# Performance work log

Hardware: AMD Instinct MI355X
Metric: run time of the kernel (lower is better)

Reference implementation:

```python
import jax, jax.numpy as jnp
import numpy as np
import math

C = 512         # embed_size
L_V = 196       # num_patches (square -> no cls token)
B_V = 64        # image batch
B_T = 32        # caption batch
N_WORD = 24     # words per caption (all cap_lens equal)
SPARSE_RATIO = 0.5
AGGR_RATIO = 0.5
NUM_KEEP = math.ceil(L_V * SPARSE_RATIO)            # 98 kept tokens
KEEPED = int(L_V * AGGR_RATIO * SPARSE_RATIO)       # 49 aggregated tokens
HIDDEN = int(C * 0.2)                               # 102 MLP hidden (dim_ratio=0.2)
LAMBDA = 4.0                                        # xattn softmax temperature
LN_EPS = 1e-5


def l2norm(x, axis=-1):
    n = jnp.linalg.norm(x, axis=axis, keepdims=True)
    return x / jnp.maximum(n, 1e-12)


def setup_inputs() -> dict:
    key = jax.random.key(0)
    ks = jax.random.split(key, 4)
    img_embs = jax.random.normal(ks[0], (B_V, L_V, C), dtype=jnp.float32)
    cap_embs = jax.random.normal(ks[1], (B_T, N_WORD, C), dtype=jnp.float32)
    cap_lens = jnp.full((B_T,), N_WORD, dtype=jnp.int64 if jax.config.read('jax_enable_x64') else jnp.int32)
    # TokenAggregation params: LayerNorm -> Linear(C,HIDDEN) -> GELU -> Linear(HIDDEN,KEEPED), scale
    ln_gamma = jnp.ones((C,), jnp.float32)
    ln_beta = jnp.zeros((C,), jnp.float32)
    W1 = jax.random.normal(ks[2], (C, HIDDEN), dtype=jnp.float32) * 0.02
    b1 = jnp.zeros((HIDDEN,), jnp.float32)
    W2 = jax.random.normal(ks[3], (HIDDEN, KEEPED), dtype=jnp.float32) * 0.02
    b2 = jnp.zeros((KEEPED,), jnp.float32)
    scale = jnp.ones((), jnp.float32)
    return dict(img_embs=img_embs, cap_embs=cap_embs, cap_lens=cap_lens,
                ln_gamma=ln_gamma, ln_beta=ln_beta, W1=W1, b1=b1, W2=W2, b2=b2, scale=scale)


def _forward(img_embs, cap_embs, ln_gamma, ln_beta, W1, b1, W2, b2, scale):
    # --- global attention scores (computed under no_grad in torch) ---
    img_norm = l2norm(img_embs)                                   # (Bv,Lv,C)
    cap_norm = l2norm(cap_embs)                                   # (Bt,W,C)
    img_glo = l2norm(jnp.mean(img_embs, axis=1, keepdims=True))   # (Bv,1,C)
    self_attn = jnp.sum(img_glo * img_norm, axis=-1)              # (Bv,Lv)
    cap_glo = l2norm(jnp.mean(cap_embs, axis=1))                  # (Bt,C)
    cross_attn = jnp.einsum('tc,vlc->tvl', cap_glo, img_norm)     # (Bt,Bv,Lv)
    score = jax.lax.stop_gradient(self_attn[None] + cross_attn)   # (Bt,Bv,Lv)

    # --- TokenSparse: sort, split keep / non-keep ---
    order = jnp.argsort(-score, axis=-1)                          # descending indices
    score_sort = jnp.take_along_axis(score, order, axis=-1)
    keep_idx = order[..., :NUM_KEEP]                              # (Bt,Bv,K)
    non_idx = order[..., NUM_KEEP:]                               # (Bt,Bv,Lv-K)
    rank = jnp.argsort(order, axis=-1)                            # inverse permutation
    score_mask = (rank < NUM_KEEP).astype(score.dtype)            # (Bt,Bv,Lv)

    bidx = jnp.arange(B_V)[None, :, None]
    select_tokens = img_embs[bidx, keep_idx]                      # (Bt,Bv,K,C) gather
    non_tokens = img_embs[bidx, non_idx]                          # (Bt,Bv,Lv-K,C)
    non_w = jax.nn.softmax(score_sort[..., NUM_KEEP:], axis=-1)   # (Bt,Bv,Lv-K)
    extra_token = jnp.sum(non_tokens * non_w[..., None], axis=-2, keepdims=True)  # (Bt,Bv,1,C)

    # --- TokenAggregation: LN -> MLP -> softmax -> bmm ---
    mu = jnp.mean(select_tokens, axis=-1, keepdims=True)
    var = jnp.var(select_tokens, axis=-1, keepdims=True)
    xn = (select_tokens - mu) * jax.lax.rsqrt(var + LN_EPS) * ln_gamma + ln_beta
    h = jax.nn.gelu(jnp.einsum('tvkc,ch->tvkh', xn, W1) + b1, approximate=False)
    w = jnp.einsum('tvkh,hp->tvkp', h, W2) + b2                   # (Bt,Bv,K,P)
    w = jnp.swapaxes(w, -1, -2) * scale                           # (Bt,Bv,P,K)
    w = jax.nn.softmax(w, axis=-1)
    aggr = jnp.einsum('tvpk,tvkc->tvpc', w, select_tokens)        # (Bt,Bv,P,C)

    keep_tokens = jnp.concatenate([aggr, extra_token], axis=2)    # (Bt,Bv,P+1,C)
    sel_norm = l2norm(keep_tokens)

    # --- mask_xattn_one_text: SCAN-style t2i attention ---
    sims = jnp.einsum('twc,tvpc->tvwp', cap_norm, sel_norm)       # (Bt,Bv,W,P+1)
    attn = jax.nn.softmax(LAMBDA * sims, axis=-1)
    ctx = l2norm(jnp.einsum('tvwp,tvpc->tvwc', attn, sel_norm))   # (Bt,Bv,W,C)
    word_sim = jnp.einsum('twc,tvwc->tvw', cap_norm, ctx)         # (Bt,Bv,W)
    sim = jnp.mean(word_sim, axis=-1)                             # (Bt,Bv)
    improve_sims = sim.T                                          # (Bv,Bt)
    return improve_sims, score_mask


def reference(img_embs, cap_embs, cap_lens, ln_gamma, ln_beta, W1, b1, W2, b2, scale):
    # cap_lens are all N_WORD (constant), so the per-caption loop is fully vectorized.
    return _forward(img_embs, cap_embs, ln_gamma, ln_beta, W1, b1, W2, b2, scale)
```

## Files before the change

### kernel.cpp

```cpp
#include <hip/hip_runtime.h>
#include <hip/hip_bf16.h>
#include <math.h>

#define CDIM 512
#define LV 196
#define BV 64
#define BT 32
#define NW 24
#define NKEEP 98
#define NNON 98
#define KEEPED 49
#define HID 102
#define LAMBDA_ 4.0f
#define LN_EPS_ 1e-5f

#define WS_CAPNORM 0
#define WS_CAPGLO  (WS_CAPNORM + BT*NW*CDIM)
#define WS_IMGGLO  (WS_CAPGLO + BT*CDIM)
#define WS_INVN    (WS_IMGGLO + BV*CDIM)
#define WS_WLOG    (WS_INVN + BV*LV)
#define WS_SCORE   (WS_WLOG + BV*LV*KEEPED)
#define WS_END     (WS_SCORE + BT*BV*LV)
#define WS_IMGT_B  ((size_t)WS_END * 4)
#define TOKPAD 224
#define WS_NEED_B  (WS_IMGT_B + (size_t)BV * CDIM * TOKPAD * 2)
#define WS_W1T_B   ((size_t)WS_SCORE * 4)
#define WS_W2T_B   (WS_W1T_B + (size_t)112 * 512 * 2)

typedef short v8s __attribute__((ext_vector_type(8)));
typedef float v4f __attribute__((ext_vector_type(4)));
#define MFMA16(a, b, c) __builtin_amdgcn_mfma_f32_16x16x32_bf16((a), (b), (c), 0, 0, 0)

#define WA_STR 232
#define TOK_STR 40
#define SEL_STR 520
#define G_STR 66
#define XN_STR 520
#define HB_STR 136

#define SELQ_STR 136
#define CAPQ_STR 136
#define K4_SMEM   51968
#define OFF_SEL   0
#define OFF_WA    19216
#define OFF_CAPQ  19216
#define OFF_SIMS  19216
#define OFF_G     27408
#define OFF_SC    48912
#define OFF_KIDX  49696
#define OFF_NIDX  50088
#define OFF_CNT   50480
#define OFF_WK    50496
#define OFF_RED   50896
#define OFF_POOL2 51408
#define OFF_INV   51664

__device__ __forceinline__ ushort bfb(float f) {
  __hip_bfloat16 h = __float2bfloat16(f);
  union { __hip_bfloat16 h; ushort u; } cv; cv.h = h; return cv.u;
}

__global__ __launch_bounds__(512) void k0_prep(const float* __restrict__ img,
                                               const float* __restrict__ W1,
                                               const float* __restrict__ W2,
                                               float* __restrict__ ws) {
  int v = blockIdx.x, kt = blockIdx.y, c = threadIdx.x;
  if (kt == 7) {
    if (v < 56) {
      #pragma unroll
      for (int r = 0; r < 2; ++r) {
        int h = v * 2 + r;
        float val = (h < HID) ? W1[(size_t)c * HID + h] : 0.f;
        ((ushort*)((char*)ws + WS_W1T_B))[(size_t)h * 512 + c] = bfb(val);
      }
    } else {
      for (int e = c; e < 1024; e += 512) {
        int idx = (v - 56) * 1024 + e;
        int p = idx >> 7, h = idx & 127;
        float val = (p < KEEPED && h < HID) ? W2[(size_t)h * KEEPED + p] : 0.f;
        ((ushort*)((char*)ws + WS_W2T_B))[(size_t)p * 128 + h] = bfb(val);
      }
    }
    return;
  }
  float x[32];
  #pragma unroll
  for (int kk = 0; kk < 32; ++kk) {
    int tok = kt * 32 + kk;
    x[kk] = (tok < LV) ? img[((size_t)v * LV + tok) * CDIM + c] : 0.f;
  }
  __hip_bfloat16* imgT = (__hip_bfloat16*)((char*)ws + WS_IMGT_B);
  uint* dst = (uint*)(imgT + ((size_t)v * CDIM + c) * TOKPAD + kt * 32);
  #pragma unroll
  for (int g = 0; g < 4; ++g) {
    uint4 u;
    u.x = (uint)bfb(x[g*8+0]) | ((uint)bfb(x[g*8+1]) << 16);
    u.y = (uint)bfb(x[g*8+2]) | ((uint)bfb(x[g*8+3]) << 16);
    u.z = (uint)bfb(x[g*8+4]) | ((uint)bfb(x[g*8+5]) << 16);
    u.w = (uint)bfb(x[g*8+6]) | ((uint)bfb(x[g*8+7]) << 16);
    *(uint4*)(dst + g * 4) = u;
  }
}

__global__ __launch_bounds__(512) void k5_prep(const float* __restrict__ W1,
                                               const float* __restrict__ W2,
                                               float* __restrict__ ws) {
  int b = blockIdx.x, tid = threadIdx.x;
  if (b < 112) {
    int h = b;
    float val = (h < HID) ? W1[(size_t)tid * HID + h] : 0.f;
    ((ushort*)((char*)ws + WS_W1T_B))[(size_t)h * 512 + tid] = bfb(val);
  } else {
    int p = b - 112;
    if (tid < 128) {
      int h = tid;
      float val = (p < KEEPED && h < HID) ? W2[(size_t)h * KEEPED + p] : 0.f;
      ((ushort*)((char*)ws + WS_W2T_B))[(size_t)p * 128 + h] = bfb(val);
    }
  }
}

__global__ __launch_bounds__(256) void k1_glo(const float* __restrict__ img,
                                              const float* __restrict__ cap,
                                              float* __restrict__ ws) {
  __shared__ float red[256];
  __shared__ float s_part[4 * CDIM];
  __shared__ float s_glo[CDIM];
  int b = blockIdx.x, tid = threadIdx.x;
  if (b < BT) {
    int t = b;
    int wv = tid >> 6, lane = tid & 63;
    int cb = lane * 8;
    float4 sA = make_float4(0.f,0.f,0.f,0.f), sB = make_float4(0.f,0.f,0.f,0.f);
    for (int w = wv; w < NW; w += 4) {
      const float* p = cap + ((size_t)t * NW + w) * CDIM + cb;
      float4 xa = *(const float4*)p;
      float4 xb = *(const float4*)(p + 4);
      float ss = xa.x*xa.x + xa.y*xa.y + xa.z*xa.z + xa.w*xa.w
               + xb.x*xb.x + xb.y*xb.y + xb.z*xb.z + xb.w*xb.w;
      #pragma unroll
      for (int off = 32; off > 0; off >>= 1) ss += __shfl_xor(ss, off, 64);
      float inv = 1.f / fmaxf(sqrtf(ss), 1e-12f);
      float* q = ws + WS_CAPNORM + ((size_t)t * NW + w) * CDIM + cb;
      *(float4*)q       = make_float4(xa.x*inv, xa.y*inv, xa.z*inv, xa.w*inv);
      *(float4*)(q + 4) = make_float4(xb.x*inv, xb.y*inv, xb.z*inv, xb.w*inv);
      sA.x += xa.x; sA.y += xa.y; sA.z += xa.z; sA.w += xa.w;
      sB.x += xb.x; sB.y += xb.y; sB.z += xb.z; sB.w += xb.w;
    }
    *(float4*)&s_part[wv * CDIM + cb]     = sA;
    *(float4*)&s_part[wv * CDIM + cb + 4] = sB;
    __syncthreads();
    if (tid < 128) {
      float4 g = make_float4(0.f, 0.f, 0.f, 0.f);
      #pragma unroll
      for (int w2 = 0; w2 < 4; ++w2) {
        float4 pv = *(const float4*)&s_part[w2 * CDIM + tid * 4];
        g.x += pv.x; g.y += pv.y; g.z += pv.z; g.w += pv.w;
      }
      g.x /= (float)NW; g.y /= (float)NW; g.z /= (float)NW; g.w /= (float)NW;
      *(float4*)&s_glo[tid * 4] = g;
      red[tid] = g.x*g.x + g.y*g.y + g.z*g.z + g.w*g.w;
    }
    __syncthreads();
    for (int off = 64; off > 0; off >>= 1) {
      if (tid < off) red[tid] += red[tid + off];
      __syncthreads();
    }
    float inv = 1.f / fmaxf(sqrtf(red[0]), 1e-12f);
    if (tid < 128) {
      float4 g = *(const float4*)&s_glo[tid * 4];
      *(float4*)(ws + WS_CAPGLO + (size_t)t * CDIM + tid * 4) =
          make_float4(g.x*inv, g.y*inv, g.z*inv, g.w*inv);
    }
  } else {
    int v = b - BT;
    int wv = tid >> 6, lane = tid & 63;
    int cb = lane * 8;
    const float* base = img + (size_t)v * LV * CDIM;
    float4 sA = make_float4(0.f,0.f,0.f,0.f), sB = make_float4(0.f,0.f,0.f,0.f);
    int l0 = wv * 49;
    for (int l = l0; l < l0 + 49; ++l) {
      const float* p = base + (size_t)l * CDIM + cb;
      float4 xa = *(const float4*)p;
      float4 xb = *(const float4*)(p + 4);
      sA.x += xa.x; sA.y += xa.y; sA.z += xa.z; sA.w += xa.w;
      sB.x += xb.x; sB.y += xb.y; sB.z += xb.z; sB.w += xb.w;
    }
    *(float4*)&s_part[wv * CDIM + cb]     = sA;
    *(float4*)&s_part[wv * CDIM + cb + 4] = sB;
    __syncthreads();
    if (tid < 128) {
      float4 g = make_float4(0.f, 0.f, 0.f, 0.f);
      #pragma unroll
      for (int w2 = 0; w2 < 4; ++w2) {
        float4 pv = *(const float4*)&s_part[w2 * CDIM + tid * 4];
        g.x += pv.x; g.y += pv.y; g.z += pv.z; g.w += pv.w;
      }
      g.x /= (float)LV; g.y /= (float)LV; g.z /= (float)LV; g.w /= (float)LV;
      *(float4*)&s_glo[tid * 4] = g;
      red[tid] = g.x*g.x + g.y*g.y + g.z*g.z + g.w*g.w;
    }
    __syncthreads();
    for (int off = 64; off > 0; off >>= 1) {
      if (tid < off) red[tid] += red[tid + off];
      __syncthreads();
    }
    float inv = 1.f / fmaxf(sqrtf(red[0]), 1e-12f);
    if (tid < 128) {
      float4 g = *(const float4*)&s_glo[tid * 4];
      *(float4*)(ws + WS_IMGGLO + (size_t)v * CDIM + tid * 4) =
          make_float4(g.x*inv, g.y*inv, g.z*inv, g.w*inv);
    }
  }
}

__global__ __launch_bounds__(512, 4) void k2_mlp(const float* __restrict__ img,
                                                 const float* __restrict__ gamma,
                                                 const float* __restrict__ beta,
                                                 const float* __restrict__ b1,
                                                 const float* __restrict__ b2,
                                                 float* __restrict__ ws) {
  __shared__ __align__(16) __hip_bfloat16 s_xn[32 * XN_STR];
  __hip_bfloat16* s_hb = s_xn;

  int v = blockIdx.x, seg = blockIdx.y;
  int l0 = seg * 28;
  int tid = threadIdx.x, wv = tid >> 6, lane = tid & 63;
  int quad = lane >> 4, l15 = lane & 15, koff = quad * 8;
  const __hip_bfloat16* W1T = (const __hip_bfloat16*)((const char*)ws + WS_W1T_B);
  const __hip_bfloat16* W2T = (const __hip_bfloat16*)((const char*)ws + WS_W2T_B);

  int cb = lane * 8;
  float4 g4a = *(const float4*)(gamma + cb);
  float4 g4b = *(const float4*)(gamma + cb + 4);
  float4 b4a = *(const float4*)(beta + cb);
  float4 b4b = *(const float4*)(beta + cb + 4);
  for (int tok = wv; tok < 28; tok += 8) {
    const float* p = img + ((size_t)v * LV + l0 + tok) * CDIM + cb;
    float4 xa = *(const float4*)p;
    float4 xb = *(const float4*)(p + 4);
    float s  = xa.x + xa.y + xa.z + xa.w + xb.x + xb.y + xb.z + xb.w;
    float sq = xa.x*xa.x + xa.y*xa.y + xa.z*xa.z + xa.w*xa.w
             + xb.x*xb.x + xb.y*xb.y + xb.z*xb.z + xb.w*xb.w;
    #pragma unroll
    for (int off = 32; off > 0; off >>= 1) { s += __shfl_xor(s, off, 64); sq += __shfl_xor(sq, off, 64); }
    float mean = s / (float)CDIM;
    float var = sq / (float)CDIM - mean * mean;
    float rstd = 1.f / sqrtf(var + LN_EPS_);
    if (lane == 0) ws[WS_INVN + (size_t)v * LV + l0 + tok] = 1.f / fmaxf(sqrtf(sq), 1e-12f);
    float f[8];
    f[0] = (xa.x - mean) * rstd * g4a.x + b4a.x;
    f[1] = (xa.y - mean) * rstd * g4a.y + b4a.y;
    f[2] = (xa.z - mean) * rstd * g4a.z + b4a.z;
    f[3] = (xa.w - mean) * rstd * g4a.w + b4a.w;
    f[4] = (xb.x - mean) * rstd * g4b.x + b4b.x;
    f[5] = (xb.y - mean) * rstd * g4b.y + b4b.y;
    f[6] = (xb.z - mean) * rstd * g4b.z + b4b.z;
    f[7] = (xb.w - mean) * rstd * g4b.w + b4b.w;
    uint4 u;
    u.x = (uint)bfb(f[0]) | ((uint)bfb(f[1]) << 16);
    u.y = (uint)bfb(f[2]) | ((uint)bfb(f[3]) << 16);
    u.z = (uint)bfb(f[4]) | ((uint)bfb(f[5]) << 16);
    u.w = (uint)bfb(f[6]) | ((uint)bfb(f[7]) << 16);
    *(uint4*)(s_xn + (size_t)tok * XN_STR + cb) = u;
  }
  __syncthreads();

  v4f c1[2];
  int mt_[2], nt_[2];
  #pragma unroll
  for (int i = 0; i < 2; ++i) {
    int idx = wv + 8 * i; if (idx > 13) idx = 13;
    mt_[i] = idx / 7; nt_[i] = idx % 7;
    c1[i] = (v4f){0.f, 0.f, 0.f, 0.f};
  }
  for (int ks = 0; ks < 16; ++ks) {
    #pragma unroll
    for (int i = 0; i < 2; ++i) {
      v8s a  = *(const v8s*)(s_xn + (size_t)(mt_[i] * 16 + l15) * XN_STR + ks * 32 + koff);
      v8s bb = *(const v8s*)(W1T + (size_t)(nt_[i] * 16 + l15) * 512 + ks * 32 + koff);
      c1[i] = MFMA16(a, bb, c1[i]);
    }
  }
  __syncthreads();

  #pragma unroll
  for (int i = 0; i < 2; ++i) {
    int idx = wv + 8 * i;
    if (idx < 14) {
      int h = nt_[i] * 16 + l15;
      float bias = (h < HID) ? b1[h] : 0.f;
      #pragma unroll
      for (int reg = 0; reg < 4; ++reg) {
        int row = mt_[i] * 16 + quad * 4 + reg;
        float x = c1[i][reg] + bias;
        float gl = (h < HID) ? 0.5f * x * (1.f + erff(x * 0.70710678118654752f)) : 0.f;
        s_hb[(size_t)row * HB_STR + h] = __float2bfloat16(gl);
      }
    }
  }
  for (int i = tid; i < 32 * 16; i += 512)
    s_hb[(size_t)(i >> 4) * HB_STR + 112 + (i & 15)] = __float2bfloat16(0.f);
  __syncthreads();

  int m2 = wv >> 2, n2 = wv & 3;
  v4f c2 = (v4f){0.f, 0.f, 0.f, 0.f};
  for (int ks = 0; ks < 4; ++ks) {
    v8s a  = *(const v8s*)(s_hb + (size_t)(m2 * 16 + l15) * HB_STR + ks * 32 + koff);
    v8s bb = *(const v8s*)(W2T + (size_t)(n2 * 16 + l15) * 128 + ks * 32 + koff);
    c2 = MFMA16(a, bb, c2);
  }
  {
    int p = n2 * 16 + l15;
    if (p < KEEPED) {
      float bias = b2[p];
      #pragma unroll
      for (int reg = 0; reg < 4; ++reg) {
        int tok = m2 * 16 + quad * 4 + reg;
        if (tok < 28)
          ws[WS_WLOG + ((size_t)v * LV + l0 + tok) * KEEPED + p] = c2[reg] + bias;
      }
    }
  }
}

__global__ __launch_bounds__(512) void k3_score(const float* __restrict__ img,
                                                float* __restrict__ ws) {
  __shared__ float qt[33 * 64];
  __shared__ float xt[64 * 65];
  __shared__ float dself[64];
  int v = blockIdx.x;
  int t0 = blockIdx.y * 64;
  int tid = threadIdx.x;
  int tloc = tid & 63, qg = tid >> 6;
  float acc[5];
  #pragma unroll
  for (int i = 0; i < 5; ++i) acc[i] = 0.f;
  const float* capglo = ws + WS_CAPGLO;
  const float* imgglo = ws + WS_IMGGLO + (size_t)v * CDIM;

  for (int ct = 0; ct < 8; ++ct) {
    for (int i = tid; i < 33 * 64; i += 512) {
      int q = i >> 6, cc = i & 63;
      qt[i] = (q < 32) ? capglo[(size_t)q * CDIM + ct * 64 + cc] : imgglo[ct * 64 + cc];
    }
    for (int i = tid; i < 64 * 64; i += 512) {
      int tok = i >> 6, cc = i & 63;
      int l = t0 + tok;
      xt[tok * 65 + cc] = (l < LV) ? img[((size_t)v * LV + l) * CDIM + ct * 64 + cc] : 0.f;
    }
    __syncthreads();
    for (int cc = 0; cc < 64; ++cc) {
      float xv = xt[tloc * 65 + cc];
      #pragma unroll
      for (int qi = 0; qi < 5; ++qi) {
        int q = qg + 8 * qi;
        if (q < 33) acc[qi] += qt[q * 64 + cc] * xv;
      }
    }
    __syncthreads();
  }
  if (qg == 0) dself[tloc] = acc[4];
  __syncthreads();
  int l = t0 + tloc;
  if (l < LV) {
    float invn = ws[WS_INVN + (size_t)v * LV + l];
    float ds = dself[tloc];
    #pragma unroll
    for (int qi = 0; qi < 5; ++qi) {
      int q = qg + 8 * qi;
      if (q < 32) ws[WS_SCORE + ((size_t)q * BV + v) * LV + l] = (acc[qi] + ds) * invn;
    }
  }
}

template<int USE_IMGT>
__global__ __launch_bounds__(512, 2) void k4_main(const float* __restrict__ img,
                                                  const float* __restrict__ scale_p,
                                                  const float* __restrict__ ws,
                                                  float* __restrict__ out) {
  __shared__ float s_sc[LV];
  __shared__ int   s_kidx[NKEEP];
  __shared__ int   s_nidx[NNON];
  __shared__ int   s_cnt[2];
  __shared__ float s_wk[NNON];
  __shared__ float s_red[128];
  __shared__ float s_pool2[64];
  __shared__ float s_inv[64];
  __shared__ __align__(16) __hip_bfloat16 s_selh[64 * SEL_STR];
  __shared__ __align__(16) __hip_bfloat16 s_wa[64 * WA_STR];
  __shared__ __align__(16) __hip_bfloat16 s_dyn[512 * TOK_STR];

  float* s_w = (float*)s_dyn;
  __hip_bfloat16* s_tok = s_dyn;
  __hip_bfloat16* s_cap = s_dyn;
  float* s_sims = (float*)s_wa;
  float* s_G = (float*)((char*)s_wa + 8192);

  int b = blockIdx.x;
  int v = b >> 5, t = b & 31;
  int tid = threadIdx.x;
  int wv = tid >> 6, lane = tid & 63;
  int quad = lane >> 4, l15 = lane & 15;
  int koff = quad * 8;

  if (tid < 2) s_cnt[tid] = 0;
  if (tid < 64) s_pool2[tid] = 0.f;
  if (tid < LV) s_sc[tid] = ws[WS_SCORE + ((size_t)t * BV + v) * LV + tid];
  {
    uint* za = (uint*)s_wa;
    for (int i = tid; i < 64 * WA_STR / 2; i += 512) za[i] = 0u;
    uint* zs = (uint*)(s_selh + 50 * SEL_STR);
    for (int i = tid; i < 14 * SEL_STR / 2; i += 512) zs[i] = 0u;
  }
  __syncthreads();

  if (tid < LV) {
    float my = s_sc[tid];
    int cnt = 0;
    for (int j = 0; j < LV; ++j) {
      float sj = s_sc[j];
      cnt += (sj > my) || (sj == my && j < tid);
    }
    bool keep = cnt < NKEEP;
    out[BV * BT + ((size_t)t * BV + v) * LV + tid] = keep ? 1.f : 0.f;
    if (keep) { int p = atomicAdd(&s_cnt[0], 1); s_kidx[p] = tid; }
    else      { int p = atomicAdd(&s_cnt[1], 1); s_nidx[p] = tid; }
  }
  __syncthreads();

  if (tid < 128) s_red[tid] = (tid < NNON) ? s_sc[s_nidx[tid]] : -3.0e38f;
  __syncthreads();
  for (int off = 64; off > 0; off >>= 1) {
    if (tid < off) s_red[tid] = fmaxf(s_red[tid], s_red[tid + off]);
    __syncthreads();
  }
  float nm = s_red[0];
  __syncthreads();
  float e0 = 0.f;
  if (tid < NNON) e0 = expf(s_sc[s_nidx[tid]] - nm);
  if (tid < 128) s_red[tid] = (tid < NNON) ? e0 : 0.f;
  __syncthreads();
  for (int off = 64; off > 0; off >>= 1) {
    if (tid < off) s_red[tid] += s_red[tid + off];
    __syncthreads();
  }
  float nS = s_red[0];
  __syncthreads();
  if (tid < NNON) s_wk[tid] = e0 / nS;
  __syncthreads();

  float scale_val = scale_p[0];
  for (int i = tid; i < KEEPED * NKEEP; i += 512) {
    int k = i / KEEPED, p = i - k * KEEPED;
    s_w[p * NKEEP + k] = ws[WS_WLOG + ((size_t)v * LV + s_kidx[k]) * KEEPED + p] * scale_val;
  }
  __syncthreads();
  if (tid < KEEPED * 8) {
    int p = tid >> 3, g = tid & 7;
    float mm = -3e38f;
    for (int k = g; k < NKEEP; k += 8) mm = fmaxf(mm, s_w[p * NKEEP + k]);
    #pragma unroll
    for (int off = 4; off > 0; off >>= 1) mm = fmaxf(mm, __shfl_xor(mm, off, 8));
    float ss = 0.f;
    for (int k = g; k < NKEEP; k += 8) {
      float ee = expf(s_w[p * NKEEP + k] - mm);
      s_w[p * NKEEP + k] = ee;
      ss += ee;
    }
    #pragma unroll
    for (int off = 4; off > 0; off >>= 1) ss += __shfl_xor(ss, off, 8);
    float rs = 1.f / ss;
    for (int k = g; k < NKEEP; k += 8) s_w[p * NKEEP + k] *= rs;
  }
  __syncthreads();

  for (int i = tid; i < KEEPED * NKEEP; i += 512) {
    int p = i / NKEEP, r = i - p * NKEEP;
    s_wa[p * WA_STR + s_kidx[r]] = __float2bfloat16(s_w[p * NKEEP + r]);
  }
  if (tid < NNON) s_wa[49 * WA_STR + s_nidx[tid]] = __float2bfloat16(s_wk[tid]);
  __syncthreads();

  v4f acc[4][4];
  #pragma unroll
  for (int m = 0; m < 4; ++m)
    #pragma unroll
    for (int j = 0; j < 4; ++j) acc[m][j] = (v4f){0.f, 0.f, 0.f, 0.f};

  if (USE_IMGT) {
    const __hip_bfloat16* imgTv =
        (const __hip_bfloat16*)((const char*)ws + WS_IMGT_B) + (size_t)v * CDIM * TOKPAD;
    for (int ks = 0; ks < 7; ++ks) {
      v8s bfr[4];
      #pragma unroll
      for (int j = 0; j < 4; ++j)
        bfr[j] = *(const v8s*)(imgTv + (size_t)(wv * 64 + j * 16 + l15) * TOKPAD + ks * 32 + koff);
      #pragma unroll
      for (int m = 0; m < 4; ++m) {
        v8s af = *(const v8s*)(s_wa + (m * 16 + l15) * WA_STR + ks * 32 + koff);
        #pragma unroll
        for (int j = 0; j < 4; ++j) acc[m][j] = MFMA16(af, bfr[j], acc[m][j]);
      }
    }
  } else {
    for (int ks = 0; ks < 7; ++ks) {
      #pragma unroll
      for (int it = 0; it < 8; ++it) {
        int k0 = ks * 32 + it * 4;
        if (k0 < LV) {
          const float* gp = img + ((size_t)v * LV + k0) * CDIM + tid;
          float x0 = gp[0], x1 = gp[CDIM], x2 = gp[2 * CDIM], x3 = gp[3 * CDIM];
          union { __hip_bfloat16 h[4]; uint2 u; } pk;
          pk.h[0] = __float2bfloat16(x0); pk.h[1] = __float2bfloat16(x1);
          pk.h[2] = __float2bfloat16(x2); pk.h[3] = __float2bfloat16(x3);
          *(uint2*)(s_tok + tid * TOK_STR + it * 4) = pk.u;
        }
      }
      __syncthreads();
      v8s bfr[4];
      #pragma unroll
      for (int j = 0; j < 4; ++j)
        bfr[j] = *(const v8s*)(s_tok + (wv * 64 + j * 16 + l15) * TOK_STR + koff);
      #pragma unroll
      for (int m = 0; m < 4; ++m) {
        v8s af = *(const v8s*)(s_wa + (m * 16 + l15) * WA_STR + ks * 32 + koff);
        #pragma unroll
        for (int j = 0; j < 4; ++j) acc[m][j] = MFMA16(af, bfr[j], acc[m][j]);
      }
      __syncthreads();
    }
  }

  if (!USE_IMGT) __syncthreads();
  for (int i = tid; i < NW * 128; i += 512) {
    int w = i >> 7, cq = i & 127;
    const float4 xv = *(const float4*)(ws + WS_CAPNORM + ((size_t)t * NW + w) * CDIM + cq * 4);
    union { __hip_bfloat16 h[4]; uint2 u; } pk;
    pk.h[0] = __float2bfloat16(xv.x); pk.h[1] = __float2bfloat16(xv.y);
    pk.h[2] = __float2bfloat16(xv.z); pk.h[3] = __float2bfloat16(xv.w);
    *(uint2*)(s_cap + w * SEL_STR + cq * 4) = pk.u;
  }
  {
    uint* zc = (uint*)(s_cap + 24 * SEL_STR);
    for (int i = tid; i < 8 * SEL_STR / 2; i += 512) zc[i] = 0u;
  }
  #pragma unroll
  for (int m = 0; m < 4; ++m) {
    #pragma unroll
    for (int reg = 0; reg < 4; ++reg) {
      float ss = acc[m][0][reg] * acc[m][0][reg] + acc[m][1][reg] * acc[m][1][reg]
               + acc[m][2][reg] * acc[m][2][reg] + acc[m][3][reg] * acc[m][3][reg];
      #pragma unroll
      for (int off = 8; off > 0; off >>= 1) ss += __shfl_xor(ss, off, 64);
      if (l15 == 0) atomicAdd(&s_pool2[m * 16 + quad * 4 + reg], ss);
    }
  }
  __syncthreads();
  if (tid < 64) s_inv[tid] = 1.f / fmaxf(sqrtf(s_pool2[tid]), 1e-12f);
  __syncthreads();
  #pragma unroll
  for (int m = 0; m < 4; ++m) {
    #pragma unroll
    for (int reg = 0; reg < 4; ++reg) {
      int p = m * 16 + quad * 4 + reg;
      if (p < 50) {
        float iv = s_inv[p];
        #pragma unroll
        for (int j = 0; j < 4; ++j)
          s_selh[p * SEL_STR + wv * 64 + j * 16 + l15] = __float2bfloat16(acc[m][j][reg] * iv);
      }
    }
  }
  __syncthreads();

  {
    int mt = wv >> 2, nt = wv & 3;
    v4f sa = (v4f){0.f, 0.f, 0.f, 0.f};
    for (int ks = 0; ks < 16; ++ks) {
      v8s a = *(const v8s*)(s_cap + (mt * 16 + l15) * SEL_STR + ks * 32 + koff);
      v8s bb = *(const v8s*)(s_selh + (nt * 16 + l15) * SEL_STR + ks * 32 + koff);
      sa = MFMA16(a, bb, sa);
    }
    #pragma unroll
    for (int reg = 0; reg < 4; ++reg)
      s_sims[(mt * 16 + quad * 4 + reg) * 64 + nt * 16 + l15] = sa[reg];
  }
  __syncthreads();

  if (tid < NW * 8) {
    int w = tid >> 3, g = tid & 7;
    float* row = s_sims + w * 64;
    float mm = -3e38f;
    for (int p = g; p < 50; p += 8) mm = fmaxf(mm, row[p]);
    #pragma unroll
    for (int off = 4; off > 0; off >>= 1) mm = fmaxf(mm, __shfl_xor(mm, off, 8));
    float num = 0.f;
    for (int p = g; p < 64; p += 8) {
      if (p < 50) {
        float s = row[p];
        float ee = expf(LAMBDA_ * (s - mm));
        num += ee * s;
        row[p] = ee;
      } else row[p] = 0.f;
    }
    #pragma unroll
    for (int off = 4; off > 0; off >>= 1) num += __shfl_xor(num, off, 8);
    if (g == 0) s_red[w] = num;
  }
  __syncthreads();

  #pragma unroll
  for (int i2 = 0; i2 < 2; ++i2) {
    int idx = wv * 2 + i2;
    int gm = idx >> 2, gn = idx & 3;
    v4f ga = (v4f){0.f, 0.f, 0.f, 0.f};
    for (int ks = 0; ks < 16; ++ks) {
      v8s a = *(const v8s*)(s_selh + (gm * 16 + l15) * SEL_STR + ks * 32 + koff);
      v8s bb = *(const v8s*)(s_selh + (gn * 16 + l15) * SEL_STR + ks * 32 + koff);
      ga = MFMA16(a, bb, ga);
    }
    #pragma unroll
    for (int reg = 0; reg < 4; ++reg)
      s_G[(gm * 16 + quad * 4 + reg) * G_STR + gn * 16 + l15] = ga[reg];
  }
  __syncthreads();

  float wacc = 0.f;
  for (int w = wv; w < NW; w += 8) {
    const float* ev = s_sims + w * 64;
    float tl = 0.f;
    for (int q = 0; q < 50; ++q) tl += s_G[q * G_STR + lane] * ev[q];
    float ql = ev[lane] * tl;
    #pragma unroll
    for (int off = 32; off > 0; off >>= 1) ql += __shfl_xor(ql, off, 64);
    if (lane == 0) wacc += s_red[w] / fmaxf(sqrtf(ql), 1e-20f);
  }
  if (lane == 0) s_red[64 + wv] = wacc;
  __syncthreads();
  if (tid == 0) {
    float s = 0.f;
    #pragma unroll
    for (int i = 0; i < 8; ++i) s += s_red[64 + i];
    out[(size_t)v * BT + t] = s / (float)NW;
  }
}

__global__ __launch_bounds__(512, 4) void k4_big(const float* __restrict__ img,
                                                 const float* __restrict__ scale_p,
                                                 const float* __restrict__ ws,
                                                 float* __restrict__ out) {
  __shared__ __align__(16) char smem[K4_SMEM];
  __hip_bfloat16* s_sel = (__hip_bfloat16*)(smem + OFF_SEL);
  float*          s_w   = (float*)(smem + OFF_SEL);
  __hip_bfloat16* s_wa  = (__hip_bfloat16*)(smem + OFF_WA);
  __hip_bfloat16* s_capq= (__hip_bfloat16*)(smem + OFF_CAPQ);
  float*          s_sims= (float*)(smem + OFF_SIMS);
  float*          s_G   = (float*)(smem + OFF_G);
  float* s_sc    = (float*)(smem + OFF_SC);
  int*   s_kidx  = (int*)(smem + OFF_KIDX);
  int*   s_nidx  = (int*)(smem + OFF_NIDX);
  int*   s_cnt   = (int*)(smem + OFF_CNT);
  float* s_wk    = (float*)(smem + OFF_WK);
  float* s_red   = (float*)(smem + OFF_RED);
  float* s_pool2 = (float*)(smem + OFF_POOL2);
  float* s_inv   = (float*)(smem + OFF_INV);

  int b0 = blockIdx.x;
  int b = ((b0 & 7) << 8) | (b0 >> 3);
  int v = b >> 5, t = b & 31;
  int tid = threadIdx.x;
  int wv = tid >> 6, lane = tid & 63;
  int quad = lane >> 4, l15 = lane & 15;
  int koff = quad * 8;

  if (tid < 2) s_cnt[tid] = 0;
  if (tid < 64) s_pool2[tid] = 0.f;
  if (tid < LV) s_sc[tid] = ws[WS_SCORE + ((size_t)t * BV + v) * LV + tid];
  {
    uint* za = (uint*)s_wa;
    for (int i = tid; i < 64 * WA_STR / 2; i += 512) za[i] = 0u;
  }
  __syncthreads();

  if (tid < LV) {
    float my = s_sc[tid];
    int cnt = 0;
    for (int j = 0; j < LV; ++j) {
      float sj = s_sc[j];
      cnt += (sj > my) || (sj == my && j < tid);
    }
    bool keep = cnt < NKEEP;
    out[BV * BT + ((size_t)t * BV + v) * LV + tid] = keep ? 1.f : 0.f;
    if (keep) { int p = atomicAdd(&s_cnt[0], 1); s_kidx[p] = tid; }
    else      { int p = atomicAdd(&s_cnt[1], 1); s_nidx[p] = tid; }
  }
  __syncthreads();

  if (tid < 128) s_red[tid] = (tid < NNON) ? s_sc[s_nidx[tid]] : -3.0e38f;
  __syncthreads();
  for (int off = 64; off > 0; off >>= 1) {
    if (tid < off) s_red[tid] = fmaxf(s_red[tid], s_red[tid + off]);
    __syncthreads();
  }
  float nm = s_red[0];
  __syncthreads();
  float e0 = 0.f;
  if (tid < NNON) e0 = expf(s_sc[s_nidx[tid]] - nm);
  if (tid < 128) s_red[tid] = (tid < NNON) ? e0 : 0.f;
  __syncthreads();
  for (int off = 64; off > 0; off >>= 1) {
    if (tid < off) s_red[tid] += s_red[tid + off];
    __syncthreads();
  }
  float nS = s_red[0];
  __syncthreads();
  if (tid < NNON) s_wk[tid] = e0 / nS;
  __syncthreads();

  float scale_val = scale_p[0];
  for (int i = tid; i < KEEPED * NKEEP; i += 512) {
    int k = i / KEEPED, p = i - k * KEEPED;
    s_w[p * NKEEP + k] = ws[WS_WLOG + ((size_t)v * LV + s_kidx[k]) * KEEPED + p] * scale_val;
  }
  __syncthreads();
  if (tid < KEEPED * 8) {
    int p = tid >> 3, g = tid & 7;
    float mm = -3e38f;
    for (int k = g; k < NKEEP; k += 8) mm = fmaxf(mm, s_w[p * NKEEP + k]);
    #pragma unroll
    for (int off = 4; off > 0; off >>= 1) mm = fmaxf(mm, __shfl_xor(mm, off, 8));
    float ss = 0.f;
    for (int k = g; k < NKEEP; k += 8) {
      float ee = expf(s_w[p * NKEEP + k] - mm);
      s_w[p * NKEEP + k] = ee;
      ss += ee;
    }
    #pragma unroll
    for (int off = 4; off > 0; off >>= 1) ss += __shfl_xor(ss, off, 8);
    float rs = 1.f / ss;
    for (int k = g; k < NKEEP; k += 8) s_w[p * NKEEP + k] *= rs;
  }
  __syncthreads();

  for (int i = tid; i < KEEPED * NKEEP; i += 512) {
    int p = i / NKEEP, r = i - p * NKEEP;
    s_wa[p * WA_STR + s_kidx[r]] = __float2bfloat16(s_w[p * NKEEP + r]);
  }
  if (tid < NNON) s_wa[49 * WA_STR + s_nidx[tid]] = __float2bfloat16(s_wk[tid]);
  __syncthreads();

  {
    uint* zq = (uint*)(s_sel + 50 * SELQ_STR);
    for (int i = tid; i < 14 * SELQ_STR / 2; i += 512) zq[i] = 0u;
  }

  v4f acc[4][4];
  #pragma unroll
  for (int m = 0; m < 4; ++m)
    #pragma unroll
    for (int j = 0; j < 4; ++j) acc[m][j] = (v4f){0.f, 0.f, 0.f, 0.f};

  {
    const __hip_bfloat16* imgTv =
        (const __hip_bfloat16*)((const char*)ws + WS_IMGT_B) + (size_t)v * CDIM * TOKPAD;
    for (int ks = 0; ks < 7; ++ks) {
      v8s bfr[4];
      #pragma unroll
      for (int j = 0; j < 4; ++j)
        bfr[j] = *(const v8s*)(imgTv + (size_t)(wv * 64 + j * 16 + l15) * TOKPAD + ks * 32 + koff);
      #pragma unroll
      for (int m = 0; m < 4; ++m) {
        v8s af = *(const v8s*)(s_wa + (m * 16 + l15) * WA_STR + ks * 32 + koff);
        #pragma unroll
        for (int j = 0; j < 4; ++j) acc[m][j] = MFMA16(af, bfr[j], acc[m][j]);
      }
    }
  }

  #pragma unroll
  for (int m = 0; m < 4; ++m) {
    #pragma unroll
    for (int reg = 0; reg < 4; ++reg) {
      float ss = acc[m][0][reg] * acc[m][0][reg] + acc[m][1][reg] * acc[m][1][reg]
               + acc[m][2][reg] * acc[m][2][reg] + acc[m][3][reg] * acc[m][3][reg];
      #pragma unroll
      for (int off = 8; off > 0; off >>= 1) ss += __shfl_xor(ss, off, 64);
      if (l15 == 0) atomicAdd(&s_pool2[m * 16 + quad * 4 + reg], ss);
    }
  }
  __syncthreads();
  if (tid < 64) s_inv[tid] = 1.f / fmaxf(sqrtf(s_pool2[tid]), 1e-12f);
  __syncthreads();

  uint pk[4][4][2];
  #pragma unroll
  for (int m = 0; m < 4; ++m) {
    #pragma unroll
    for (int rp = 0; rp < 2; ++rp) {
      int p0 = m * 16 + quad * 4 + rp * 2;
      float iv0 = s_inv[p0], iv1 = s_inv[p0 + 1];
      #pragma unroll
      for (int j = 0; j < 4; ++j)
        pk[m][j][rp] = (uint)bfb(acc[m][j][2 * rp] * iv0)
                     | ((uint)bfb(acc[m][j][2 * rp + 1] * iv1) << 16);
    }
  }

  v4f sa = (v4f){0.f, 0.f, 0.f, 0.f};
  v4f ga[2];
  ga[0] = (v4f){0.f, 0.f, 0.f, 0.f};
  ga[1] = (v4f){0.f, 0.f, 0.f, 0.f};
  ushort* selw = (ushort*)s_sel;
  int mt = wv >> 2, nt = wv & 3;
  for (int q = 0; q < 4; ++q) {
    if ((wv >> 1) == q) {
      int base = (wv & 1) * 64;
      #pragma unroll
      for (int m = 0; m < 4; ++m) {
        #pragma unroll
        for (int reg = 0; reg < 4; ++reg) {
          int p = m * 16 + quad * 4 + reg;
          if (p < 50) {
            #pragma unroll
            for (int j = 0; j < 4; ++j) {
              uint u = pk[m][j][reg >> 1];
              ushort val = (reg & 1) ? (ushort)(u >> 16) : (ushort)(u & 0xffffu);
              selw[p * SELQ_STR + base + j * 16 + l15] = val;
            }
          }
        }
      }
    } else {
      int rank = wv - (wv > 2 * q + 1 ? 2 : 0);
      int lt = rank * 64 + lane;
      for (int i = lt; i < NW * 32; i += 384) {
        int w = i >> 5, c4 = i & 31;
        float4 xv = *(const float4*)(ws + WS_CAPNORM + ((size_t)t * NW + w) * CDIM
                                     + q * 128 + c4 * 4);
        union { __hip_bfloat16 hh[4]; uint2 u; } pc;
        pc.hh[0] = __float2bfloat16(xv.x); pc.hh[1] = __float2bfloat16(xv.y);
        pc.hh[2] = __float2bfloat16(xv.z); pc.hh[3] = __float2bfloat16(xv.w);
        *(uint2*)(s_capq + w * CAPQ_STR + c4 * 4) = pc.u;
      }
    }
    __syncthreads();
    #pragma unroll
    for (int ks = 0; ks < 4; ++ks) {
      v8s a  = *(const v8s*)(s_capq + (mt * 16 + l15) * CAPQ_STR + ks * 32 + koff);
      v8s bb = *(const v8s*)(s_sel + (nt * 16 + l15) * SELQ_STR + ks * 32 + koff);
      sa = MFMA16(a, bb, sa);
    }
    #pragma unroll
    for (int i2 = 0; i2 < 2; ++i2) {
      int idx = wv * 2 + i2;
      int gm = idx >> 2, gn = idx & 3;
      #pragma unroll
      for (int ks = 0; ks < 4; ++ks) {
        v8s a  = *(const v8s*)(s_sel + (gm * 16 + l15) * SELQ_STR + ks * 32 + koff);
        v8s bb = *(const v8s*)(s_sel + (gn * 16 + l15) * SELQ_STR + ks * 32 + koff);
        ga[i2] = MFMA16(a, bb, ga[i2]);
      }
    }
    __syncthreads();
  }

  #pragma unroll
  for (int reg = 0; reg < 4; ++reg)
    s_sims[(mt * 16 + quad * 4 + reg) * 64 + nt * 16 + l15] = sa[reg];
  #pragma unroll
  for (int i2 = 0; i2 < 2; ++i2) {
    int idx = wv * 2 + i2;
    int gm = idx >> 2, gn = idx & 3;
    #pragma unroll
    for (int reg = 0; reg < 4; ++reg)
      s_G[(gm * 16 + quad * 4 + reg) * G_STR + gn * 16 + l15] = ga[i2][reg];
  }
  __syncthreads();

  if (tid < NW * 8) {
    int w = tid >> 3, g = tid & 7;
    float* row = s_sims + w * 64;
    float mm = -3e38f;
    for (int p = g; p < 50; p += 8) mm = fmaxf(mm, row[p]);
    #pragma unroll
    for (int off = 4; off > 0; off >>= 1) mm = fmaxf(mm, __shfl_xor(mm, off, 8));
    float num = 0.f;
    for (int p = g; p < 64; p += 8) {
      if (p < 50) {
        float s = row[p];
        float ee = expf(LAMBDA_ * (s - mm));
        num += ee * s;
        row[p] = ee;
      } else row[p] = 0.f;
    }
    #pragma unroll
    for (int off = 4; off > 0; off >>= 1) num += __shfl_xor(num, off, 8);
    if (g == 0) s_red[w] = num;
  }
  __syncthreads();

  float wacc = 0.f;
  for (int w = wv; w < NW; w += 8) {
    const float* ev = s_sims + w * 64;
    float tl = 0.f;
    for (int q = 0; q < 50; ++q) tl += s_G[q * G_STR + lane] * ev[q];
    float ql = ev[lane] * tl;
    #pragma unroll
    for (int off = 32; off > 0; off >>= 1) ql += __shfl_xor(ql, off, 64);
    if (lane == 0) wacc += s_red[w] / fmaxf(sqrtf(ql), 1e-20f);
  }
  if (lane == 0) s_red[64 + wv] = wacc;
  __syncthreads();
  if (tid == 0) {
    float s = 0.f;
    #pragma unroll
    for (int i = 0; i < 8; ++i) s += s_red[64 + i];
    out[(size_t)v * BT + t] = s / (float)NW;
  }
}

extern "C" void kernel_launch(void* const* d_in, const int* in_sizes, int n_in,
                              void* d_out, int out_size, void* d_ws, size_t ws_size,
                              hipStream_t stream) {
  const float* img   = (const float*)d_in[0];
  const float* cap   = (const float*)d_in[1];
  const float* gamma = (const float*)d_in[3];
  const float* beta  = (const float*)d_in[4];
  const float* W1    = (const float*)d_in[5];
  const float* b1    = (const float*)d_in[6];
  const float* W2    = (const float*)d_in[7];
  const float* b2    = (const float*)d_in[8];
  const float* scale = (const float*)d_in[9];
  float* ws  = (float*)d_ws;
  float* out = (float*)d_out;

  const bool big = (ws_size >= WS_NEED_B);

  if (big) k0_prep<<<dim3(BV, 8), dim3(512), 0, stream>>>(img, W1, W2, ws);
  else     k5_prep<<<dim3(176), dim3(512), 0, stream>>>(W1, W2, ws);
  k1_glo <<<dim3(BT + BV), dim3(256), 0, stream>>>(img, cap, ws);
  k2_mlp <<<dim3(BV, 7), dim3(512), 0, stream>>>(img, gamma, beta, b1, b2, ws);
  k3_score<<<dim3(BV, 4), dim3(512), 0, stream>>>(img, ws);
  if (big) k4_big<<<dim3(BV * BT), dim3(512), 0, stream>>>(img, scale, ws, out);
  else     k4_main<0><<<dim3(BV * BT), dim3(512), 0, stream>>>(img, scale, ws, out);
}
```

Baseline: 347.0 us.

## Fuse image mean partials into transpose prep, vectorize score LDS, shuffle reductions

The prep kernel that transposes images now also writes per-tile column sums into the workspace region later used for MLP logits. In the big-workspace path, the global-feature kernel reduces those partials instead of re-reading the full image tensor. The score kernel reads its LDS tiles as float2 with a padded stride, and the softmax max/sum over non-kept tokens uses wavefront shuffles instead of shared-memory tree reductions with many barriers. Reusing the logits region for the partials depends on k2 running after k1, and it adds scattered global writes to the prep kernel.

```diff
diff --git a/kernel.cpp b/kernel.cpp
--- a/kernel.cpp
+++ b/kernel.cpp
@@ -26,6 +26,7 @@
 #define WS_NEED_B  (WS_IMGT_B + (size_t)BV * CDIM * TOKPAD * 2)
 #define WS_W1T_B   ((size_t)WS_SCORE * 4)
 #define WS_W2T_B   (WS_W1T_B + (size_t)112 * 512 * 2)
+#define WS_IPART   WS_WLOG
 
 typedef short v8s __attribute__((ext_vector_type(8)));
 typedef float v4f __attribute__((ext_vector_type(4)));
@@ -89,6 +90,12 @@
     int tok = kt * 32 + kk;
     x[kk] = (tok < LV) ? img[((size_t)v * LV + tok) * CDIM + c] : 0.f;
   }
+  {
+    float s = 0.f;
+    #pragma unroll
+    for (int kk = 0; kk < 32; ++kk) s += x[kk];
+    ws[WS_IPART + ((size_t)kt * BV + v) * CDIM + c] = s;
+  }
   __hip_bfloat16* imgT = (__hip_bfloat16*)((char*)ws + WS_IMGT_B);
   uint* dst = (uint*)(imgT + ((size_t)v * CDIM + c) * TOKPAD + kt * 32);
   #pragma unroll
@@ -120,6 +127,7 @@
   }
 }
 
+template<int BIG>
 __global__ __launch_bounds__(256) void k1_glo(const float* __restrict__ img,
                                               const float* __restrict__ cap,
                                               float* __restrict__ ws) {
@@ -172,6 +180,25 @@
       *(float4*)(ws + WS_CAPGLO + (size_t)t * CDIM + tid * 4) =
           make_float4(g.x*inv, g.y*inv, g.z*inv, g.w*inv);
     }
+  } else if (BIG) {
+    int v = b - BT;
+    int c0 = tid, c1 = tid + 256;
+    float s0 = 0.f, s1 = 0.f;
+    #pragma unroll
+    for (int kt = 0; kt < 7; ++kt) {
+      s0 += ws[WS_IPART + ((size_t)kt * BV + v) * CDIM + c0];
+      s1 += ws[WS_IPART + ((size_t)kt * BV + v) * CDIM + c1];
+    }
+    float g0 = s0 / (float)LV, g1 = s1 / (float)LV;
+    red[tid] = g0 * g0 + g1 * g1;
+    __syncthreads();
+    for (int off = 128; off > 0; off >>= 1) {
+      if (tid < off) red[tid] += red[tid + off];
+      __syncthreads();
+    }
+    float inv = 1.f / fmaxf(sqrtf(red[0]), 1e-12f);
+    float* q = ws + WS_IMGGLO + (size_t)v * CDIM;
+    q[c0] = g0 * inv; q[c1] = g1 * inv;
   } else {
     int v = b - BT;
     int wv = tid >> 6, lane = tid & 63;
@@ -326,8 +353,8 @@
 
 __global__ __launch_bounds__(512) void k3_score(const float* __restrict__ img,
                                                 float* __restrict__ ws) {
-  __shared__ float qt[33 * 64];
-  __shared__ float xt[64 * 65];
+  __shared__ __align__(16) float qt[33 * 64];
+  __shared__ __align__(16) float xt[64 * 66];
   __shared__ float dself[64];
   int v = blockIdx.x;
   int t0 = blockIdx.y * 64;
@@ -347,15 +374,19 @@
     for (int i = tid; i < 64 * 64; i += 512) {
       int tok = i >> 6, cc = i & 63;
       int l = t0 + tok;
-      xt[tok * 65 + cc] = (l < LV) ? img[((size_t)v * LV + l) * CDIM + ct * 64 + cc] : 0.f;
-    }
-    __syncthreads();
-    for (int cc = 0; cc < 64; ++cc) {
-      float xv = xt[tloc * 65 + cc];
+      xt[tok * 66 + cc] = (l < LV) ? img[((size_t)v * LV + l) * CDIM + ct * 64 + cc] : 0.f;
+    }
+    __syncthreads();
+    for (int cc2 = 0; cc2 < 32; ++cc2) {
+      float2 xv = *(const float2*)&xt[tloc * 66 + cc2 * 2];
       #pragma unroll
       for (int qi = 0; qi < 5; ++qi) {
         int q = qg + 8 * qi;
-        if (q < 33) acc[qi] += qt[q * 64 + cc] * xv;
+        if (q < 33) {
+          float2 qv = *(const float2*)&qt[q * 64 + cc2 * 2];
+          acc[qi] += qv.x * xv.x;
+          acc[qi] += qv.y * xv.y;
+        }
       }
     }
     __syncthreads();
@@ -697,24 +728,24 @@
   }
   __syncthreads();
 
-  if (tid < 128) s_red[tid] = (tid < NNON) ? s_sc[s_nidx[tid]] : -3.0e38f;
-  __syncthreads();
-  for (int off = 64; off > 0; off >>= 1) {
-    if (tid < off) s_red[tid] = fmaxf(s_red[tid], s_red[tid + off]);
-    __syncthreads();
-  }
-  float nm = s_red[0];
-  __syncthreads();
+  if (tid < 128) {
+    float vmax = (tid < NNON) ? s_sc[s_nidx[tid]] : -3.0e38f;
+    #pragma unroll
+    for (int off = 32; off > 0; off >>= 1) vmax = fmaxf(vmax, __shfl_xor(vmax, off, 64));
+    if ((tid & 63) == 0) s_red[tid >> 6] = vmax;
+  }
+  __syncthreads();
+  float nm = fmaxf(s_red[0], s_red[1]);
   float e0 = 0.f;
-  if (tid < NNON) e0 = expf(s_sc[s_nidx[tid]] - nm);
-  if (tid < 128) s_red[tid] = (tid < NNON) ? e0 : 0.f;
-  __syncthreads();
-  for (int off = 64; off > 0; off >>= 1) {
-    if (tid < off) s_red[tid] += s_red[tid + off];
-    __syncthreads();
-  }
-  float nS = s_red[0];
-  __syncthreads();
+  if (tid < 128) {
+    float vs = 0.f;
+    if (tid < NNON) { e0 = expf(s_sc[s_nidx[tid]] - nm); vs = e0; }
+    #pragma unroll
+    for (int off = 32; off > 0; off >>= 1) vs += __shfl_xor(vs, off, 64);
+    if ((tid & 63) == 0) s_red[2 + (tid >> 6)] = vs;
+  }
+  __syncthreads();
+  float nS = s_red[2] + s_red[3];
   if (tid < NNON) s_wk[tid] = e0 / nS;
   __syncthreads();
 
@@ -937,9 +968,13 @@
 
   const bool big = (ws_size >= WS_NEED_B);
 
-  if (big) k0_prep<<<dim3(BV, 8), dim3(512), 0, stream>>>(img, W1, W2, ws);
-  else     k5_prep<<<dim3(176), dim3(512), 0, stream>>>(W1, W2, ws);
-  k1_glo <<<dim3(BT + BV), dim3(256), 0, stream>>>(img, cap, ws);
+  if (big) {
+    k0_prep<<<dim3(BV, 8), dim3(512), 0, stream>>>(img, W1, W2, ws);
+    k1_glo<1><<<dim3(BT + BV), dim3(256), 0, stream>>>(img, cap, ws);
+  } else {
+    k5_prep<<<dim3(176), dim3(512), 0, stream>>>(W1, W2, ws);
+    k1_glo<0><<<dim3(BT + BV), dim3(256), 0, stream>>>(img, cap, ws);
+  }
   k2_mlp <<<dim3(BV, 7), dim3(512), 0, stream>>>(img, gamma, beta, b1, b2, ws);
   k3_score<<<dim3(BV, 4), dim3(512), 0, stream>>>(img, ws);
   if (big) k4_big<<<dim3(BV * BT), dim3(512), 0, stream>>>(img, scale, ws, out);
```

Result: faster. 303.2 us (-12.6%).
